# Kernel tuning notes

Hardware: AMD Instinct MI355X
Metric: run time of the kernel (lower is better)

The kernel has to match this reference:

```python
import jax, jax.numpy as jnp
import numpy as np
from jax import lax

B, L = 16, 2048
D_TOK, D_TIS = 256, 64
D_MODEL = D_TOK + D_TIS          # 320
EXPAND = 2
D_INNER = EXPAND * D_MODEL       # 640
D_STATE = 16
D_CONV = 4
DT_RANK = (D_MODEL + 15) // 16   # 20 (ceil(d_model/16), Mamba default)
H_OUT = 128
VOCAB = 65                       # len(CODON_MAP_DNA)+1
N_TISSUES = 30
MAX_NORM = 2.0


def _embed_maxnorm(W, idx):
    # torch nn.Embedding(max_norm=2): looked-up rows are renormalized to norm<=2
    e = W[idx]
    n = jnp.linalg.norm(e, axis=-1, keepdims=True)
    return e * jnp.minimum(1.0, MAX_NORM / jnp.maximum(n, 1e-12))


def setup_inputs() -> dict:
    key = jax.random.key(0)
    ks = jax.random.split(key, 18)
    s = 0.02
    seq_W = jax.random.normal(ks[3], (VOCAB, D_TOK), dtype=jnp.float32)
    seq_W = seq_W.at[0].set(0.0)  # padding_idx=0
    A_log = jnp.log(jnp.broadcast_to(jnp.arange(1, D_STATE + 1, dtype=jnp.float32), (D_INNER, D_STATE)))
    return {
        "rna_data_pad": jax.random.randint(ks[0], (B, L), 0, VOCAB).astype(jnp.int32),
        "tissue_id": jax.random.randint(ks[1], (B,), 0, N_TISSUES).astype(jnp.int32),
        "seq_lengths": jax.random.randint(ks[2], (B,), 1, L + 1).astype(jnp.int32),
        "seq_W": seq_W,
        "tissue_W": jax.random.normal(ks[4], (N_TISSUES, D_TIS), dtype=jnp.float32),
        "in_proj_W": jax.random.normal(ks[5], (2 * D_INNER, D_MODEL), dtype=jnp.float32) * s,
        "conv_w": jax.random.normal(ks[6], (D_INNER, 1, D_CONV), dtype=jnp.float32) * s,
        "conv_b": jnp.zeros((D_INNER,), dtype=jnp.float32),
        "x_proj_W": jax.random.normal(ks[7], (DT_RANK + 2 * D_STATE, D_INNER), dtype=jnp.float32) * s,
        "dt_proj_W": jax.random.normal(ks[8], (D_INNER, DT_RANK), dtype=jnp.float32) * s,
        "dt_proj_b": jax.random.uniform(ks[9], (D_INNER,), minval=-4.0, maxval=-2.0),
        "A_log": A_log,
        "D_skip": jnp.ones((D_INNER,), dtype=jnp.float32),
        "out_proj_W": jax.random.normal(ks[10], (D_MODEL, D_INNER), dtype=jnp.float32) * s,
        "p1_W": jax.random.normal(ks[11], (H_OUT, D_MODEL), dtype=jnp.float32) * s,
        "p1_b": jnp.zeros((H_OUT,), dtype=jnp.float32),
        "p2_W": jax.random.normal(ks[12], (1, H_OUT), dtype=jnp.float32) * s,
        "p2_b": jnp.zeros((1,), dtype=jnp.float32),
    }


def reference(rna_data_pad, tissue_id, seq_lengths, seq_W, tissue_W, in_proj_W,
              conv_w, conv_b, x_proj_W, dt_proj_W, dt_proj_b, A_log, D_skip,
              out_proj_W, p1_W, p1_b, p2_W, p2_b):
    b, l = rna_data_pad.shape
    # embeddings + tissue broadcast + mask
    seq_emb = _embed_maxnorm(seq_W, rna_data_pad)            # [B,L,D_TOK]
    tis_emb = _embed_maxnorm(tissue_W, tissue_id)            # [B,D_TIS]
    tis_exp = jnp.broadcast_to(tis_emb[:, None, :], (b, l, tis_emb.shape[-1]))
    x = jnp.concatenate([seq_emb, tis_exp], axis=-1)          # [B,L,D_MODEL]
    x = x * (rna_data_pad != 0)[..., None]
    # Mamba block
    xz = x @ in_proj_W.T                                      # [B,L,2*D_INNER]
    xm, z = jnp.split(xz, 2, axis=-1)
    xt = xm.transpose(0, 2, 1)                                # [B,D_INNER,L]
    conv = lax.conv_general_dilated(
        xt, conv_w, window_strides=(1,), padding=[(D_CONV - 1, 0)],
        feature_group_count=D_INNER,
        dimension_numbers=("NCH", "OIH", "NCH")) + conv_b[None, :, None]
    xm = jax.nn.silu(conv).transpose(0, 2, 1)                 # [B,L,D_INNER]
    x_dbl = xm @ x_proj_W.T                                   # [B,L,DT_RANK+2*D_STATE]
    dt, Bm, Cm = jnp.split(x_dbl, [DT_RANK, DT_RANK + D_STATE], axis=-1)
    delta = jax.nn.softplus(dt @ dt_proj_W.T + dt_proj_b)     # [B,L,D_INNER]
    A = -jnp.exp(A_log)                                       # [D_INNER,D_STATE]
    # selective scan over time
    xs = (delta.transpose(1, 0, 2), Bm.transpose(1, 0, 2),
          Cm.transpose(1, 0, 2), xm.transpose(1, 0, 2))
    h0 = jnp.zeros((b, D_INNER, D_STATE), dtype=xm.dtype)

    def step(h, t):
        dl, bt, ct, ut = t                                    # [B,di],[B,ds],[B,ds],[B,di]
        dA = jnp.exp(dl[:, :, None] * A)                      # [B,di,ds]
        dBu = (dl * ut)[:, :, None] * bt[:, None, :]          # [B,di,ds]
        h = dA * h + dBu
        y = jnp.einsum("bds,bs->bd", h, ct)
        return h, y

    _, ys = lax.scan(step, h0, xs)                            # ys: [L,B,D_INNER]
    y = ys.transpose(1, 0, 2) + xm * D_skip
    y = y * jax.nn.silu(z)
    out = y @ out_proj_W.T                                    # [B,L,D_MODEL]
    # gather last valid timestep
    out_last = out[jnp.arange(b), seq_lengths - 1]            # [B,D_MODEL]
    h1 = jax.nn.relu(out_last @ p1_W.T + p1_b)
    return h1 @ p2_W.T + p2_b                                 # [B,1]
```

## Files before the change

### kernel.cpp

```cpp
#include <hip/hip_runtime.h>
#include <hip/hip_bf16.h>
#include <hip/hip_fp16.h>
#include <math.h>

#define B_      16
#define L_      2048
#define D_MODEL 320
#define D_INNER 640
#define D_STATE 16
#define DT_RANK 20
#define H_OUT   128
#define VOCAB   65
#define N_TIS   30
#define TT      8
#define ST      64
#define NCHUNK  16
#define CHLEN   (L_/NCHUNK)

static constexpr size_t OFF_MSEQ  = 0;
static constexpr size_t OFF_MTIS  = OFF_MSEQ + VOCAB*1280;
static constexpr size_t OFF_YSCAN = OFF_MTIS + N_TIS*1280;
static constexpr size_t OFF_CLAST = OFF_YSCAN + B_*D_INNER;
static constexpr size_t OFF_XD20  = OFF_CLAST + B_*16;
static constexpr size_t OFF_BBAR  = OFF_XD20 + (size_t)B_*L_*20;
static constexpr size_t OFF_PC    = OFF_BBAR + (size_t)B_*D_STATE*L_;
static constexpr size_t OFF_SC    = OFF_PC + (size_t)B_*NCHUNK*40*256;
static constexpr size_t OFF_U     = OFF_SC + (size_t)B_*NCHUNK*40*256;
static constexpr size_t WS_NEED_BYTES = OFF_U*4 + (size_t)B_*L_*D_INNER*2;

__device__ __forceinline__ float fast_rcp(float x) { return __builtin_amdgcn_rcpf(x); }
__device__ __forceinline__ float silu_f(float x) { return x * fast_rcp(1.0f + __expf(-x)); }

__global__ __launch_bounds__(256) void k_mbuild(
    const float* __restrict__ seqW, const float* __restrict__ tisW,
    const float* __restrict__ inW, float* __restrict__ ws)
{
    __shared__ float a_l[256];
    __shared__ float red[4];
    int v = blockIdx.x, tid = threadIdx.x;
    int K, wofs; const float* src; float* dstM;
    if (v < VOCAB) { K = 256; wofs = 0;   src = seqW + (size_t)v*256;        dstM = ws + OFF_MSEQ + (size_t)v*1280; }
    else           { K = 64;  wofs = 256; src = tisW + (size_t)(v-VOCAB)*64; dstM = ws + OFF_MTIS + (size_t)(v-VOCAB)*1280; }
    float x = (tid < K) ? src[tid] : 0.0f;
    float ss = x * x;
    #pragma unroll
    for (int o = 32; o; o >>= 1) ss += __shfl_xor(ss, o);
    if ((tid & 63) == 0) red[tid >> 6] = ss;
    __syncthreads();
    float tot = red[0] + red[1] + red[2] + red[3];
    float scale = fminf(1.0f, 2.0f / fmaxf(sqrtf(tot), 1e-12f));
    a_l[tid] = (tid < K) ? x * scale : 0.0f;
    __syncthreads();

    int wv = tid >> 6, l = tid & 63;
    float4 a4 = ((const float4*)a_l)[l];
    int j0 = blockIdx.y * 256 + wv * 64;
    bool lane_on = (4*l < K);
    for (int jj = 0; jj < 64; jj += 4) {
        float p[4];
        #pragma unroll
        for (int u = 0; u < 4; ++u) {
            float pv = 0.0f;
            if (lane_on) {
                const float4 w4 = *(const float4*)(inW + (size_t)(j0 + jj + u)*320 + wofs + 4*l);
                pv = a4.x*w4.x + a4.y*w4.y + a4.z*w4.z + a4.w*w4.w;
            }
            p[u] = pv;
        }
        float ta, tb;
        ta=__shfl_xor(p[0],1); tb=__shfl_xor(p[1],1); p[0]=(l&1)?(p[1]+tb):(p[0]+ta);
        ta=__shfl_xor(p[2],1); tb=__shfl_xor(p[3],1); p[2]=(l&1)?(p[3]+tb):(p[2]+ta);
        ta=__shfl_xor(p[0],2); tb=__shfl_xor(p[2],2); p[0]=(l&2)?(p[2]+tb):(p[0]+ta);
        p[0]+=__shfl_xor(p[0],4);  p[0]+=__shfl_xor(p[0],8);
        p[0]+=__shfl_xor(p[0],16); p[0]+=__shfl_xor(p[0],32);
        if (l < 4) dstM[j0 + jj + l] = p[0];
    }
}

__global__ __launch_bounds__(256) void k_xdbl(
    const int* __restrict__ idx, const int* __restrict__ tissue_id,
    const int* __restrict__ seq_lengths,
    const float* __restrict__ conv_w, const float* __restrict__ conv_b,
    const float* __restrict__ xW, float* __restrict__ ws, int use_u)
{
    __shared__ float u_l[TT*641];
    __shared__ float xd_l[TT*36];
    __shared__ int   idx_l[TT+3];
    int b = blockIdx.y;
    int t0 = blockIdx.x * TT;
    int t_last = seq_lengths[b] - 1;
    if (t0 > t_last) return;
    int tid = threadIdx.x;
    const float* Mseq = ws + OFF_MSEQ;
    const float* Mtis = ws + OFF_MTIS;
    int tis = tissue_id[b];
    if (tid < TT+3) {
        int t = t0 - 3 + tid;
        idx_l[tid] = (t >= 0) ? idx[b*L_ + t] : 0;
    }
    __syncthreads();

    for (int d = tid; d < D_INNER; d += 256) {
        float w0 = conv_w[d*4+0], w1 = conv_w[d*4+1], w2 = conv_w[d*4+2], w3 = conv_w[d*4+3];
        float cb = conv_b[d];
        float mt = Mtis[(size_t)tis*1280 + d];
        float xzv[TT+3];
        #pragma unroll
        for (int k = 0; k < TT+3; ++k) {
            unsigned ro = (unsigned)idx_l[k] * 1280u;
            xzv[k] = ro ? (Mseq[ro + (unsigned)d] + mt) : 0.0f;
        }
        #pragma unroll
        for (int t = 0; t < TT; ++t) {
            float c = cb;
            c = fmaf(w0, xzv[t+0], c);
            c = fmaf(w1, xzv[t+1], c);
            c = fmaf(w2, xzv[t+2], c);
            c = fmaf(w3, xzv[t+3], c);
            u_l[t*641 + d] = silu_f(c);
        }
    }
    __syncthreads();

    if (use_u) {
        int nt = min(TT, t_last - t0 + 1);
        __half* Ub = (__half*)(ws + OFF_U) + ((size_t)b*L_ + t0)*D_INNER;
        int cnt = nt * D_INNER;
        for (int o = tid; o < cnt; o += 256) {
            int t = o / D_INNER, d = o - t*D_INNER;
            Ub[o] = __float2half(u_l[t*641 + d]);
        }
    }

    {
        int w = tid >> 6, l = tid & 63;
        float wreg[9][10];
        #pragma unroll
        for (int kk = 0; kk < 9; ++kk) {
            const float* xr = xW + (size_t)(w + 4*kk)*D_INNER + l;
            #pragma unroll
            for (int i = 0; i < 10; ++i) wreg[kk][i] = xr[64*i];
        }
        for (int t = 0; t < TT; ++t) {
            float p[9];
            #pragma unroll
            for (int kk = 0; kk < 9; ++kk) p[kk] = 0.f;
            #pragma unroll
            for (int i = 0; i < 10; ++i) {
                float ui = u_l[t*641 + l + 64*i];
                #pragma unroll
                for (int kk = 0; kk < 9; ++kk) p[kk] = fmaf(wreg[kk][i], ui, p[kk]);
            }
            {
                float ta, tb;
                ta=__shfl_xor(p[0],1); tb=__shfl_xor(p[1],1); p[0]=(l&1)?(p[1]+tb):(p[0]+ta);
                ta=__shfl_xor(p[2],1); tb=__shfl_xor(p[3],1); p[2]=(l&1)?(p[3]+tb):(p[2]+ta);
                ta=__shfl_xor(p[4],1); tb=__shfl_xor(p[5],1); p[4]=(l&1)?(p[5]+tb):(p[4]+ta);
                ta=__shfl_xor(p[6],1); tb=__shfl_xor(p[7],1); p[6]=(l&1)?(p[7]+tb):(p[6]+ta);
                p[8]+=__shfl_xor(p[8],1);
                ta=__shfl_xor(p[0],2); tb=__shfl_xor(p[2],2); p[0]=(l&2)?(p[2]+tb):(p[0]+ta);
                ta=__shfl_xor(p[4],2); tb=__shfl_xor(p[6],2); p[4]=(l&2)?(p[6]+tb):(p[4]+ta);
                p[8]+=__shfl_xor(p[8],2);
                ta=__shfl_xor(p[0],4); tb=__shfl_xor(p[4],4); p[0]=(l&4)?(p[4]+tb):(p[0]+ta);
                p[8]+=__shfl_xor(p[8],4);
                ta=__shfl_xor(p[0],8); tb=__shfl_xor(p[8],8); p[0]=(l&8)?(p[8]+tb):(p[0]+ta);
                p[0]+=__shfl_xor(p[0],16);
                p[0]+=__shfl_xor(p[0],32);
            }
            if (l < 9) xd_l[t*36 + w + 4*l] = p[0];
        }
        if (t_last < t0 + TT) {
            int tl = t_last - t0;
            float pc[4];
            #pragma unroll
            for (int k = 0; k < 4; ++k) pc[k] = 0.f;
            #pragma unroll
            for (int i = 0; i < 10; ++i) {
                float ui = u_l[tl*641 + l + 64*i];
                #pragma unroll
                for (int k = 0; k < 4; ++k)
                    pc[k] = fmaf(xW[(size_t)(36 + w + 4*k)*D_INNER + l + 64*i], ui, pc[k]);
            }
            #pragma unroll
            for (int o = 32; o; o >>= 1) {
                #pragma unroll
                for (int k = 0; k < 4; ++k) pc[k] += __shfl_xor(pc[k], o);
            }
            if (l == 0) {
                #pragma unroll
                for (int k = 0; k < 4; ++k) ws[OFF_CLAST + b*16 + w + 4*k] = pc[k];
            }
        }
    }
    __syncthreads();

    {
        int nt = min(TT, t_last - t0 + 1);
        int cnt = nt * 20;
        float* dst = ws + OFF_XD20 + ((size_t)b*L_ + t0)*20;
        for (int o = tid; o < cnt; o += 256) {
            int t = o / 20, r = o - t*20;
            dst[o] = xd_l[t*36 + r];
        }
        int cntB = nt * 16;
        if (tid < cntB) {
            int s, tt;
            if (nt == TT) { s = tid >> 3; tt = tid & 7; }
            else          { s = tid / nt; tt = tid - s*nt; }
            ws[OFF_BBAR + ((size_t)b*D_STATE + s)*L_ + t0 + tt] = xd_l[tt*36 + 20 + s];
        }
    }
}

__global__ __launch_bounds__(256) void k_scanc(
    const int* __restrict__ idx, const int* __restrict__ tissue_id,
    const int* __restrict__ seq_lengths,
    const float* __restrict__ conv_w, const float* __restrict__ conv_b,
    const float* __restrict__ dtW, const float* __restrict__ dtb,
    const float* __restrict__ A_log, float* __restrict__ ws, int use_u)
{
    __shared__ float xd_t[ST*20];
    __shared__ float dl_t[16*68];
    __shared__ float du_t[16*68];
    __shared__ float Bb_t[16*68];
    __shared__ float sdred[16*17];
    __shared__ int   idx_t[ST+3];

    int dg = blockIdx.x, b = blockIdx.y, c = blockIdx.z;
    int t_last = seq_lengths[b] - 1;
    int t_begin = c * CHLEN;
    if (t_begin > t_last) return;
    int t_end = min(t_begin + CHLEN - 1, t_last);
    int tid = threadIdx.x;
    int dl = tid >> 4, s = tid & 15;
    int dd = tid & 15, tg = tid >> 4;
    int d_own = dg*16 + dd;
    unsigned dco = (unsigned)d_own;
    int tis = tissue_id[b];
    const float* Mseq = ws + OFF_MSEQ;

    float dtw_r[20];
    #pragma unroll
    for (int i = 0; i < 20; i += 4) {
        float4 w4 = *(const float4*)(dtW + d_own*20 + i);
        dtw_r[i] = w4.x; dtw_r[i+1] = w4.y; dtw_r[i+2] = w4.z; dtw_r[i+3] = w4.w;
    }
    float4 cw4 = make_float4(0.f,0.f,0.f,0.f);
    float  cb = 0.f, mt = 0.f;
    if (!use_u) {
        cw4 = *(const float4*)(conv_w + d_own*4);
        cb  = conv_b[d_own];
        mt  = ws[OFF_MTIS + (size_t)tis*1280 + d_own];
    }
    float  dtb_v = dtb[d_own];
    float As = -__expf(A_log[(dg*16 + dl)*D_STATE + s]) * 1.44269504089f;

    float h = 0.0f;
    float sdp = 0.0f;
    for (int t0 = t_begin; t0 <= t_end; t0 += ST) {
        int nt = min(ST, t_end - t0 + 1);
        if (!use_u && tid < ST+3) {
            int t = t0 - 3 + tid;
            idx_t[tid] = (t >= 0 && t < L_) ? idx[b*L_ + t] : 0;
        }
        {
            const float4* src = (const float4*)(ws + OFF_XD20 + ((size_t)b*L_ + t0)*20);
            float4* dst = (float4*)xd_t;
            int cnt4 = nt * 5;
            for (int o = tid; o < cnt4; o += 256) dst[o] = src[o];
        }
        {
            int lr = tid >> 4, c4 = (tid & 15) * 4;
            if (c4 < nt)
                *(float4*)(Bb_t + lr*68 + c4) =
                    *(const float4*)(ws + OFF_BBAR + ((size_t)b*D_STATE + lr)*L_ + t0 + c4);
        }
        __syncthreads();

        {
            int ttb = tg * 4;
            if (ttb < nt) {
                float uu[4];
                if (use_u) {
                    const __half* Ub = (const __half*)(ws + OFF_U)
                                     + ((size_t)b*L_ + t0 + ttb)*D_INNER + dco;
                    #pragma unroll
                    for (int j = 0; j < 4; ++j)
                        uu[j] = (ttb + j < nt) ? __half2float(Ub[(size_t)j*D_INNER]) : 0.0f;
                } else {
                    float xz[7];
                    #pragma unroll
                    for (int k = 0; k < 7; ++k) {
                        unsigned ro = (unsigned)idx_t[ttb + k] * 1280u;
                        xz[k] = ro ? (Mseq[ro + dco] + mt) : 0.0f;
                    }
                    #pragma unroll
                    for (int j = 0; j < 4; ++j) {
                        float cc = cb;
                        cc = fmaf(cw4.x, xz[j+0], cc);
                        cc = fmaf(cw4.y, xz[j+1], cc);
                        cc = fmaf(cw4.z, xz[j+2], cc);
                        cc = fmaf(cw4.w, xz[j+3], cc);
                        uu[j] = (ttb + j < nt) ? silu_f(cc) : 0.0f;
                    }
                }
                float dl4[4], du4[4];
                bool full = (ttb + 3 < nt);
                #pragma unroll
                for (int j = 0; j < 4; ++j) {
                    int tt = ttb + j;
                    if (full || tt < nt) {
                        const float* xr = xd_t + tt*20;
                        float x = dtb_v;
                        #pragma unroll
                        for (int r = 0; r < 20; r += 4) {
                            float4 x4 = *(const float4*)(xr + r);
                            x = fmaf(x4.x, dtw_r[r+0], x);
                            x = fmaf(x4.y, dtw_r[r+1], x);
                            x = fmaf(x4.z, dtw_r[r+2], x);
                            x = fmaf(x4.w, dtw_r[r+3], x);
                        }
                        float e = __expf(-fabsf(x));
                        float sp = fmaxf(x, 0.0f) + __logf(1.0f + e);
                        dl4[j] = sp;
                        du4[j] = sp * uu[j];
                        sdp += sp;
                    } else { dl4[j] = 0.f; du4[j] = 0.f; }
                }
                if (full) {
                    *(float4*)(dl_t + dd*68 + ttb) = make_float4(dl4[0], dl4[1], dl4[2], dl4[3]);
                    *(float4*)(du_t + dd*68 + ttb) = make_float4(du4[0], du4[1], du4[2], du4[3]);
                } else {
                    for (int j = 0; j < 4 && ttb + j < nt; ++j) {
                        dl_t[dd*68 + ttb + j] = dl4[j];
                        du_t[dd*68 + ttb + j] = du4[j];
                    }
                }
            }
        }
        __syncthreads();

        {
            int q4 = nt >> 2;
            #pragma unroll 8
            for (int q = 0; q < q4; ++q) {
                float4 d4 = *(const float4*)(dl_t + dl*68 + 4*q);
                float4 u4 = *(const float4*)(du_t + dl*68 + 4*q);
                float4 b4 = *(const float4*)(Bb_t + s*68 + 4*q);
                float e0 = exp2f(d4.x*As), e1 = exp2f(d4.y*As);
                float e2 = exp2f(d4.z*As), e3 = exp2f(d4.w*As);
                float c0 = u4.x*b4.x, c1 = u4.y*b4.y;
                float c2 = u4.z*b4.z, c3 = u4.w*b4.w;
                h = fmaf(e0, h, c0); h = fmaf(e1, h, c1);
                h = fmaf(e2, h, c2); h = fmaf(e3, h, c3);
            }
            for (int tt = q4*4; tt < nt; ++tt) {
                float dlt = dl_t[dl*68 + tt];
                h = fmaf(exp2f(dlt * As), h, du_t[dl*68 + tt] * Bb_t[s*68 + tt]);
            }
        }
        __syncthreads();
    }
    sdred[tg*17 + dd] = sdp;
    __syncthreads();
    float sd = 0.0f;
    #pragma unroll
    for (int g = 0; g < 16; ++g) sd += sdred[g*17 + dl];
    float P = exp2f(As * sd);
    size_t base = (((size_t)b*NCHUNK + c)*40 + dg)*256 + tid;
    ws[OFF_PC + base] = P;
    ws[OFF_SC + base] = h;
}

__global__ __launch_bounds__(256) void k_comb(const int* __restrict__ seq_lengths,
                                              float* __restrict__ ws)
{
    int b = blockIdx.y, dg = blockIdx.x;
    int tid = threadIdx.x;
    int dl = tid >> 4, s = tid & 15;
    int t_last = seq_lengths[b] - 1;
    int ncv = t_last / CHLEN + 1;
    float h = 0.0f;
    for (int c = 0; c < ncv; ++c) {
        size_t base = (((size_t)b*NCHUNK + c)*40 + dg)*256 + tid;
        h = fmaf(ws[OFF_PC + base], h, ws[OFF_SC + base]);
    }
    float v = h * ws[OFF_CLAST + b*16 + s];
    v += __shfl_xor(v, 1); v += __shfl_xor(v, 2);
    v += __shfl_xor(v, 4); v += __shfl_xor(v, 8);
    if (s == 0) ws[OFF_YSCAN + (size_t)b*D_INNER + dg*16 + dl] = v;
}

__global__ __launch_bounds__(1024) void k_final(
    const int* __restrict__ idx, const int* __restrict__ tissue_id,
    const int* __restrict__ seq_lengths,
    const float* __restrict__ conv_w, const float* __restrict__ conv_b,
    const float* __restrict__ Dskip, const float* __restrict__ outW,
    const float* __restrict__ p1W, const float* __restrict__ p1b,
    const float* __restrict__ p2W, const float* __restrict__ p2b,
    const float* __restrict__ ws, float* __restrict__ out)
{
    __shared__ float y_l[D_INNER];
    __shared__ float o_l[D_MODEL];
    __shared__ float h1_l[H_OUT];
    int b = blockIdx.x, tid = threadIdx.x;
    int t_last = seq_lengths[b] - 1;
    int tis = tissue_id[b];
    const float* Mseq = ws + OFF_MSEQ;
    const float* Mtis = ws + OFF_MTIS;
    int rows[4];
    #pragma unroll
    for (int k = 0; k < 4; ++k) {
        int t = t_last - 3 + k;
        rows[k] = (t >= 0) ? idx[b*L_ + t] : 0;
    }
    if (tid < D_INNER) {
        int d = tid;
        float conv = conv_b[d];
        const float* cw = conv_w + d*4;
        #pragma unroll
        for (int k = 0; k < 4; ++k) {
            unsigned ro = (unsigned)rows[k] * 1280u;
            float xzv = ro ? (Mseq[ro + (unsigned)d] + Mtis[(size_t)tis*1280 + d]) : 0.0f;
            conv += cw[k] * xzv;
        }
        float u = silu_f(conv);
        unsigned roL = (unsigned)rows[3] * 1280u;
        float z = roL ? (Mseq[roL + 640u + (unsigned)d] + Mtis[(size_t)tis*1280 + 640 + d]) : 0.0f;
        float ys = ws[OFF_YSCAN + (size_t)b*D_INNER + d];
        y_l[d] = (ys + u * Dskip[d]) * silu_f(z);
    }
    __syncthreads();
    {
        int j = tid >> 1, half = tid & 1;
        float acc = 0.f;
        if (j < D_MODEL) {
            const float* w = outW + (size_t)j*D_INNER + half*320;
            const float* y = y_l + half*320;
            #pragma unroll 4
            for (int k = 0; k < 320; k += 4) {
                float4 w4 = *(const float4*)(w + k);
                acc += y[k]*w4.x + y[k+1]*w4.y + y[k+2]*w4.z + y[k+3]*w4.w;
            }
        }
        acc += __shfl_xor(acc, 1);
        if (j < D_MODEL && half == 0) o_l[j] = acc;
    }
    __syncthreads();
    {
        int j = tid >> 3, part = tid & 7;
        float acc = 0.f;
        if (j < H_OUT) {
            const float* w = p1W + (size_t)j*D_MODEL + part*40;
            const float* o = o_l + part*40;
            #pragma unroll
            for (int k = 0; k < 40; k += 4) {
                float4 w4 = *(const float4*)(w + k);
                acc += o[k]*w4.x + o[k+1]*w4.y + o[k+2]*w4.z + o[k+3]*w4.w;
            }
        }
        acc += __shfl_xor(acc, 1); acc += __shfl_xor(acc, 2); acc += __shfl_xor(acc, 4);
        if (j < H_OUT && part == 0) h1_l[j] = fmaxf(acc + p1b[j], 0.0f);
    }
    __syncthreads();
    if (tid < 64) {
        float v = h1_l[tid]*p2W[tid] + h1_l[tid+64]*p2W[tid+64];
        v += __shfl_xor(v, 32); v += __shfl_xor(v, 16); v += __shfl_xor(v, 8);
        v += __shfl_xor(v, 4);  v += __shfl_xor(v, 2);  v += __shfl_xor(v, 1);
        if (tid == 0) out[b] = v + p2b[0];
    }
}

extern "C" void kernel_launch(void* const* d_in, const int* in_sizes, int n_in,
                              void* d_out, int out_size, void* d_ws, size_t ws_size,
                              hipStream_t stream)
{
    const int*   idx   = (const int*)d_in[0];
    const int*   tis   = (const int*)d_in[1];
    const int*   slen  = (const int*)d_in[2];
    const float* seqW  = (const float*)d_in[3];
    const float* tisW  = (const float*)d_in[4];
    const float* inW   = (const float*)d_in[5];
    const float* convw = (const float*)d_in[6];
    const float* convb = (const float*)d_in[7];
    const float* xW    = (const float*)d_in[8];
    const float* dtW   = (const float*)d_in[9];
    const float* dtb   = (const float*)d_in[10];
    const float* Alog  = (const float*)d_in[11];
    const float* Dsk   = (const float*)d_in[12];
    const float* outW  = (const float*)d_in[13];
    const float* p1W   = (const float*)d_in[14];
    const float* p1b   = (const float*)d_in[15];
    const float* p2W   = (const float*)d_in[16];
    const float* p2b   = (const float*)d_in[17];
    float* ws  = (float*)d_ws;
    float* out = (float*)d_out;

    int use_u = (ws_size >= WS_NEED_BYTES) ? 1 : 0;

    hipLaunchKernelGGL(k_mbuild, dim3(VOCAB + N_TIS, 5), dim3(256), 0, stream, seqW, tisW, inW, ws);
    hipLaunchKernelGGL(k_xdbl,   dim3(L_/TT, B_),        dim3(256), 0, stream,
                       idx, tis, slen, convw, convb, xW, ws, use_u);
    hipLaunchKernelGGL(k_scanc,  dim3(D_INNER/16, B_, NCHUNK), dim3(256), 0, stream,
                       idx, tis, slen, convw, convb, dtW, dtb, Alog, ws, use_u);
    hipLaunchKernelGGL(k_comb,   dim3(D_INNER/16, B_),   dim3(256), 0, stream, slen, ws);
    hipLaunchKernelGGL(k_final,  dim3(B_),               dim3(1024), 0, stream,
                       idx, tis, slen, convw, convb, Dsk, outW, p1W, p1b, p2W, p2b, ws, out);
}
```

Measured before the change: 244.8 us.

## Add reverse-time closed-form scan exploiting A=-(1..16) structure with runtime check

Adds a check kernel that verifies A_log rows equal log(1..16). When it passes, a new per-channel scan kernel runs instead of the old one. The new kernel walks each chunk backwards from its end and weights contributions by integer powers of exp(-cumulative delta), so no per-state exponentials or cross-thread reductions are needed. The combine step rebuilds per-state decays from the same powers. The fp16 u buffer path is removed and B is also stored time-major; the general path remains as a fallback at the cost of an extra launch and extra flag-dependent kernel launches.

```diff
diff --git a/kernel.cpp b/kernel.cpp
--- a/kernel.cpp
+++ b/kernel.cpp
@@ -1,6 +1,5 @@
 #include <hip/hip_runtime.h>
 #include <hip/hip_bf16.h>
-#include <hip/hip_fp16.h>
 #include <math.h>
 
 #define B_      16
@@ -16,20 +15,46 @@
 #define ST      64
 #define NCHUNK  16
 #define CHLEN   (L_/NCHUNK)
+#define NCH2    32
+#define CHL2    (L_/NCH2)
 
 static constexpr size_t OFF_MSEQ  = 0;
-static constexpr size_t OFF_MTIS  = OFF_MSEQ + VOCAB*1280;
-static constexpr size_t OFF_YSCAN = OFF_MTIS + N_TIS*1280;
+static constexpr size_t OFF_MTIS  = OFF_MSEQ  + VOCAB*1280;
+static constexpr size_t OFF_YSCAN = OFF_MTIS  + N_TIS*1280;
 static constexpr size_t OFF_CLAST = OFF_YSCAN + B_*D_INNER;
-static constexpr size_t OFF_XD20  = OFF_CLAST + B_*16;
+static constexpr size_t OFF_FLAG  = OFF_CLAST + B_*16;
+static constexpr size_t OFF_XD20  = OFF_FLAG  + 16;
 static constexpr size_t OFF_BBAR  = OFF_XD20 + (size_t)B_*L_*20;
-static constexpr size_t OFF_PC    = OFF_BBAR + (size_t)B_*D_STATE*L_;
-static constexpr size_t OFF_SC    = OFF_PC + (size_t)B_*NCHUNK*40*256;
-static constexpr size_t OFF_U     = OFF_SC + (size_t)B_*NCHUNK*40*256;
-static constexpr size_t WS_NEED_BYTES = OFF_U*4 + (size_t)B_*L_*D_INNER*2;
+static constexpr size_t OFF_BT    = OFF_BBAR + (size_t)B_*D_STATE*L_;
+static constexpr size_t OFF_PC    = OFF_BT   + (size_t)B_*L_*D_STATE;
+static constexpr size_t OFF_SC    = OFF_PC   + (size_t)B_*NCHUNK*40*256;
+static constexpr size_t OFF_PCN   = OFF_SC   + (size_t)B_*NCHUNK*40*256;
+static constexpr size_t OFF_SCN   = OFF_PCN  + (size_t)B_*NCH2*D_INNER;
 
 __device__ __forceinline__ float fast_rcp(float x) { return __builtin_amdgcn_rcpf(x); }
 __device__ __forceinline__ float silu_f(float x) { return x * fast_rcp(1.0f + __expf(-x)); }
+
+__global__ __launch_bounds__(256) void k_check(const float* __restrict__ A_log,
+                                               float* __restrict__ ws)
+{
+    __shared__ int oksh;
+    int tid = threadIdx.x;
+    if (tid == 0) oksh = 1;
+    __syncthreads();
+    int ok = 1;
+    for (int i = tid; i < D_INNER*D_STATE; i += 256) {
+        int s = i & 15;
+        float v = A_log[i];
+        if (v != A_log[s]) ok = 0;
+        if (i < 16) {
+            float a = __expf(v);
+            if (fabsf(a - (float)(s+1)) > 1e-3f*(float)(s+1)) ok = 0;
+        }
+    }
+    if (!ok) atomicAnd(&oksh, 0);
+    __syncthreads();
+    if (tid == 0) ((int*)ws)[OFF_FLAG] = oksh;
+}
 
 __global__ __launch_bounds__(256) void k_mbuild(
     const float* __restrict__ seqW, const float* __restrict__ tisW,
@@ -81,7 +106,7 @@
     const int* __restrict__ idx, const int* __restrict__ tissue_id,
     const int* __restrict__ seq_lengths,
     const float* __restrict__ conv_w, const float* __restrict__ conv_b,
-    const float* __restrict__ xW, float* __restrict__ ws, int use_u)
+    const float* __restrict__ xW, float* __restrict__ ws)
 {
     __shared__ float u_l[TT*641];
     __shared__ float xd_l[TT*36];
@@ -121,16 +146,6 @@
         }
     }
     __syncthreads();
-
-    if (use_u) {
-        int nt = min(TT, t_last - t0 + 1);
-        __half* Ub = (__half*)(ws + OFF_U) + ((size_t)b*L_ + t0)*D_INNER;
-        int cnt = nt * D_INNER;
-        for (int o = tid; o < cnt; o += 256) {
-            int t = o / D_INNER, d = o - t*D_INNER;
-            Ub[o] = __float2half(u_l[t*641 + d]);
-        }
-    }
 
     {
         int w = tid >> 6, l = tid & 63;
@@ -209,7 +224,119 @@
             else          { s = tid / nt; tt = tid - s*nt; }
             ws[OFF_BBAR + ((size_t)b*D_STATE + s)*L_ + t0 + tt] = xd_l[tt*36 + 20 + s];
         }
-    }
+        for (int o = tid; o < cntB; o += 256) {
+            int t = o >> 4, s = o & 15;
+            ws[OFF_BT + ((size_t)b*L_ + t0 + t)*16 + s] = xd_l[t*36 + 20 + s];
+        }
+    }
+}
+
+__global__ __launch_bounds__(128) void k_scan2(
+    const int* __restrict__ idx, const int* __restrict__ tissue_id,
+    const int* __restrict__ seq_lengths,
+    const float* __restrict__ conv_w, const float* __restrict__ conv_b,
+    const float* __restrict__ dtW, const float* __restrict__ dtb,
+    float* __restrict__ ws)
+{
+    if (((const int*)ws)[OFF_FLAG] == 0) return;
+    int b = blockIdx.y, c = blockIdx.z;
+    int t_last = seq_lengths[b] - 1;
+    int t_begin = c * CHL2;
+    if (t_begin > t_last) return;
+    int t_end = min(t_begin + CHL2 - 1, t_last);
+    int d = blockIdx.x * 128 + threadIdx.x;
+    unsigned du = (unsigned)d;
+    int tis = tissue_id[b];
+    const float* Mseq = ws + OFF_MSEQ;
+    const float* xd   = ws + OFF_XD20 + (size_t)b*L_*20;
+    const float* BT   = ws + OFF_BT   + (size_t)b*L_*16;
+    const int*   idxb = idx + b*L_;
+
+    float dtw_r[20];
+    #pragma unroll
+    for (int i = 0; i < 20; i += 4) {
+        float4 w4 = *(const float4*)(dtW + d*20 + i);
+        dtw_r[i] = w4.x; dtw_r[i+1] = w4.y; dtw_r[i+2] = w4.z; dtw_r[i+3] = w4.w;
+    }
+    float4 cw4 = *(const float4*)(conv_w + d*4);
+    float  cb  = conv_b[d];
+    float  dtb_v = dtb[d];
+    float  mt  = ws[OFF_MTIS + (size_t)tis*1280 + d];
+    const float L2E = 1.44269504089f;
+
+    float xw0, xw1, xw2, xw3;
+    {
+        int t;
+        t = t_end;     { int row = idxb[t]; xw3 = row ? (Mseq[(unsigned)row*1280u + du] + mt) : 0.f; }
+        t = t_end - 1; { float v = 0.f; if (t >= 0) { int row = idxb[t]; v = row ? (Mseq[(unsigned)row*1280u + du] + mt) : 0.f; } xw2 = v; }
+        t = t_end - 2; { float v = 0.f; if (t >= 0) { int row = idxb[t]; v = row ? (Mseq[(unsigned)row*1280u + du] + mt) : 0.f; } xw1 = v; }
+        t = t_end - 3; { float v = 0.f; if (t >= 0) { int row = idxb[t]; v = row ? (Mseq[(unsigned)row*1280u + du] + mt) : 0.f; } xw0 = v; }
+    }
+
+    float h[16];
+    #pragma unroll
+    for (int s = 0; s < 16; ++s) h[s] = 0.f;
+    float r = 0.f;
+
+    for (int t = t_end; t >= t_begin; --t) {
+        float cc = cb;
+        cc = fmaf(cw4.x, xw0, cc);
+        cc = fmaf(cw4.y, xw1, cc);
+        cc = fmaf(cw4.z, xw2, cc);
+        cc = fmaf(cw4.w, xw3, cc);
+        float u = silu_f(cc);
+        const float4* xr4 = (const float4*)(xd + (size_t)t*20);
+        float x = dtb_v;
+        #pragma unroll
+        for (int q = 0; q < 5; ++q) {
+            float4 x4 = xr4[q];
+            x = fmaf(x4.x, dtw_r[4*q+0], x);
+            x = fmaf(x4.y, dtw_r[4*q+1], x);
+            x = fmaf(x4.z, dtw_r[4*q+2], x);
+            x = fmaf(x4.w, dtw_r[4*q+3], x);
+        }
+        float e  = __expf(-fabsf(x));
+        float dl = fmaxf(x, 0.0f) + __logf(1.0f + e);
+        float F  = dl * u;
+        float p1 = exp2f(-L2E * r);
+        float p2 = p1*p1, p3 = p2*p1, p4 = p2*p2;
+        float p5 = p4*p1, p6 = p4*p2, p7 = p4*p3, p8 = p4*p4;
+        float p9 = p8*p1, p10 = p8*p2, p11 = p8*p3, p12 = p8*p4;
+        float p13 = p8*p5, p14 = p8*p6, p15 = p8*p7, p16 = p8*p8;
+        const float4* Bt4 = (const float4*)(BT + (size_t)t*16);
+        float4 B0 = Bt4[0], B1 = Bt4[1], B2 = Bt4[2], B3 = Bt4[3];
+        h[0]  = fmaf(F*B0.x, p1,  h[0]);
+        h[1]  = fmaf(F*B0.y, p2,  h[1]);
+        h[2]  = fmaf(F*B0.z, p3,  h[2]);
+        h[3]  = fmaf(F*B0.w, p4,  h[3]);
+        h[4]  = fmaf(F*B1.x, p5,  h[4]);
+        h[5]  = fmaf(F*B1.y, p6,  h[5]);
+        h[6]  = fmaf(F*B1.z, p7,  h[6]);
+        h[7]  = fmaf(F*B1.w, p8,  h[7]);
+        h[8]  = fmaf(F*B2.x, p9,  h[8]);
+        h[9]  = fmaf(F*B2.y, p10, h[9]);
+        h[10] = fmaf(F*B2.z, p11, h[10]);
+        h[11] = fmaf(F*B2.w, p12, h[11]);
+        h[12] = fmaf(F*B3.x, p13, h[12]);
+        h[13] = fmaf(F*B3.y, p14, h[13]);
+        h[14] = fmaf(F*B3.z, p15, h[14]);
+        h[15] = fmaf(F*B3.w, p16, h[15]);
+        r += dl;
+        xw3 = xw2; xw2 = xw1; xw1 = xw0;
+        {
+            int tn = t - 4;
+            float v = 0.f;
+            if (tn >= 0) { int row = idxb[tn]; v = row ? (Mseq[(unsigned)row*1280u + du] + mt) : 0.f; }
+            xw0 = v;
+        }
+    }
+
+    ws[OFF_PCN + ((size_t)b*NCH2 + c)*D_INNER + d] = exp2f(-L2E * r);
+    float* dst = ws + OFF_SCN + (((size_t)b*NCH2 + c)*D_INNER + d)*16;
+    ((float4*)dst)[0] = make_float4(h[0],  h[1],  h[2],  h[3]);
+    ((float4*)dst)[1] = make_float4(h[4],  h[5],  h[6],  h[7]);
+    ((float4*)dst)[2] = make_float4(h[8],  h[9],  h[10], h[11]);
+    ((float4*)dst)[3] = make_float4(h[12], h[13], h[14], h[15]);
 }
 
 __global__ __launch_bounds__(256) void k_scanc(
@@ -217,8 +344,9 @@
     const int* __restrict__ seq_lengths,
     const float* __restrict__ conv_w, const float* __restrict__ conv_b,
     const float* __restrict__ dtW, const float* __restrict__ dtb,
-    const float* __restrict__ A_log, float* __restrict__ ws, int use_u)
-{
+    const float* __restrict__ A_log, float* __restrict__ ws)
+{
+    if (((const int*)ws)[OFF_FLAG] != 0) return;
     __shared__ float xd_t[ST*20];
     __shared__ float dl_t[16*68];
     __shared__ float du_t[16*68];
@@ -245,21 +373,17 @@
         float4 w4 = *(const float4*)(dtW + d_own*20 + i);
         dtw_r[i] = w4.x; dtw_r[i+1] = w4.y; dtw_r[i+2] = w4.z; dtw_r[i+3] = w4.w;
     }
-    float4 cw4 = make_float4(0.f,0.f,0.f,0.f);
-    float  cb = 0.f, mt = 0.f;
-    if (!use_u) {
-        cw4 = *(const float4*)(conv_w + d_own*4);
-        cb  = conv_b[d_own];
-        mt  = ws[OFF_MTIS + (size_t)tis*1280 + d_own];
-    }
+    float4 cw4 = *(const float4*)(conv_w + d_own*4);
+    float  cb  = conv_b[d_own];
     float  dtb_v = dtb[d_own];
+    float  mt  = ws[OFF_MTIS + (size_t)tis*1280 + d_own];
     float As = -__expf(A_log[(dg*16 + dl)*D_STATE + s]) * 1.44269504089f;
 
     float h = 0.0f;
     float sdp = 0.0f;
     for (int t0 = t_begin; t0 <= t_end; t0 += ST) {
         int nt = min(ST, t_end - t0 + 1);
-        if (!use_u && tid < ST+3) {
+        if (tid < ST+3) {
             int t = t0 - 3 + tid;
             idx_t[tid] = (t >= 0 && t < L_) ? idx[b*L_ + t] : 0;
         }
@@ -280,29 +404,11 @@
         {
             int ttb = tg * 4;
             if (ttb < nt) {
-                float uu[4];
-                if (use_u) {
-                    const __half* Ub = (const __half*)(ws + OFF_U)
-                                     + ((size_t)b*L_ + t0 + ttb)*D_INNER + dco;
-                    #pragma unroll
-                    for (int j = 0; j < 4; ++j)
-                        uu[j] = (ttb + j < nt) ? __half2float(Ub[(size_t)j*D_INNER]) : 0.0f;
-                } else {
-                    float xz[7];
-                    #pragma unroll
-                    for (int k = 0; k < 7; ++k) {
-                        unsigned ro = (unsigned)idx_t[ttb + k] * 1280u;
-                        xz[k] = ro ? (Mseq[ro + dco] + mt) : 0.0f;
-                    }
-                    #pragma unroll
-                    for (int j = 0; j < 4; ++j) {
-                        float cc = cb;
-                        cc = fmaf(cw4.x, xz[j+0], cc);
-                        cc = fmaf(cw4.y, xz[j+1], cc);
-                        cc = fmaf(cw4.z, xz[j+2], cc);
-                        cc = fmaf(cw4.w, xz[j+3], cc);
-                        uu[j] = (ttb + j < nt) ? silu_f(cc) : 0.0f;
-                    }
+                float xz[7];
+                #pragma unroll
+                for (int k = 0; k < 7; ++k) {
+                    unsigned ro = (unsigned)idx_t[ttb + k] * 1280u;
+                    xz[k] = ro ? (Mseq[ro + dco] + mt) : 0.0f;
                 }
                 float dl4[4], du4[4];
                 bool full = (ttb + 3 < nt);
@@ -310,20 +416,26 @@
                 for (int j = 0; j < 4; ++j) {
                     int tt = ttb + j;
                     if (full || tt < nt) {
+                        float cc = cb;
+                        cc = fmaf(cw4.x, xz[j+0], cc);
+                        cc = fmaf(cw4.y, xz[j+1], cc);
+                        cc = fmaf(cw4.z, xz[j+2], cc);
+                        cc = fmaf(cw4.w, xz[j+3], cc);
+                        float u = silu_f(cc);
                         const float* xr = xd_t + tt*20;
                         float x = dtb_v;
                         #pragma unroll
-                        for (int r = 0; r < 20; r += 4) {
-                            float4 x4 = *(const float4*)(xr + r);
-                            x = fmaf(x4.x, dtw_r[r+0], x);
-                            x = fmaf(x4.y, dtw_r[r+1], x);
-                            x = fmaf(x4.z, dtw_r[r+2], x);
-                            x = fmaf(x4.w, dtw_r[r+3], x);
+                        for (int rr = 0; rr < 20; rr += 4) {
+                            float4 x4 = *(const float4*)(xr + rr);
+                            x = fmaf(x4.x, dtw_r[rr+0], x);
+                            x = fmaf(x4.y, dtw_r[rr+1], x);
+                            x = fmaf(x4.z, dtw_r[rr+2], x);
+                            x = fmaf(x4.w, dtw_r[rr+3], x);
                         }
                         float e = __expf(-fabsf(x));
                         float sp = fmaxf(x, 0.0f) + __logf(1.0f + e);
                         dl4[j] = sp;
-                        du4[j] = sp * uu[j];
+                        du4[j] = sp * u;
                         sdp += sp;
                     } else { dl4[j] = 0.f; du4[j] = 0.f; }
                 }
@@ -379,11 +491,29 @@
     int tid = threadIdx.x;
     int dl = tid >> 4, s = tid & 15;
     int t_last = seq_lengths[b] - 1;
-    int ncv = t_last / CHLEN + 1;
+    int flag = ((const int*)ws)[OFF_FLAG];
     float h = 0.0f;
-    for (int c = 0; c < ncv; ++c) {
-        size_t base = (((size_t)b*NCHUNK + c)*40 + dg)*256 + tid;
-        h = fmaf(ws[OFF_PC + base], h, ws[OFF_SC + base]);
+    if (flag) {
+        int d = dg*16 + dl;
+        int n = s + 1;
+        int ncv = t_last / CHL2 + 1;
+        for (int c = 0; c < ncv; ++c) {
+            float Es = ws[OFF_PCN + ((size_t)b*NCH2 + c)*D_INNER + d];
+            float e2 = Es*Es, e4 = e2*e2, e8 = e4*e4, e16 = e8*e8;
+            float W = (n & 1) ? Es : 1.0f;
+            W *= (n & 2)  ? e2  : 1.0f;
+            W *= (n & 4)  ? e4  : 1.0f;
+            W *= (n & 8)  ? e8  : 1.0f;
+            W *= (n & 16) ? e16 : 1.0f;
+            float Sc = ws[OFF_SCN + (((size_t)b*NCH2 + c)*D_INNER + d)*16 + s];
+            h = fmaf(W, h, Sc);
+        }
+    } else {
+        int ncv = t_last / CHLEN + 1;
+        for (int c = 0; c < ncv; ++c) {
+            size_t base = (((size_t)b*NCHUNK + c)*40 + dg)*256 + tid;
+            h = fmaf(ws[OFF_PC + base], h, ws[OFF_SC + base]);
+        }
     }
     float v = h * ws[OFF_CLAST + b*16 + s];
     v += __shfl_xor(v, 1); v += __shfl_xor(v, 2);
@@ -496,13 +626,14 @@
     float* ws  = (float*)d_ws;
     float* out = (float*)d_out;
 
-    int use_u = (ws_size >= WS_NEED_BYTES) ? 1 : 0;
-
+    hipLaunchKernelGGL(k_check,  dim3(1),               dim3(256), 0, stream, Alog, ws);
     hipLaunchKernelGGL(k_mbuild, dim3(VOCAB + N_TIS, 5), dim3(256), 0, stream, seqW, tisW, inW, ws);
     hipLaunchKernelGGL(k_xdbl,   dim3(L_/TT, B_),        dim3(256), 0, stream,
-                       idx, tis, slen, convw, convb, xW, ws, use_u);
+                       idx, tis, slen, convw, convb, xW, ws);
+    hipLaunchKernelGGL(k_scan2,  dim3(D_INNER/128, B_, NCH2), dim3(128), 0, stream,
+                       idx, tis, slen, convw, convb, dtW, dtb, ws);
     hipLaunchKernelGGL(k_scanc,  dim3(D_INNER/16, B_, NCHUNK), dim3(256), 0, stream,
-                       idx, tis, slen, convw, convb, dtW, dtb, Alog, ws, use_u);
+                       idx, tis, slen, convw, convb, dtW, dtb, Alog, ws);
     hipLaunchKernelGGL(k_comb,   dim3(D_INNER/16, B_),   dim3(256), 0, stream, slen, ws);
     hipLaunchKernelGGL(k_final,  dim3(B_),               dim3(1024), 0, stream,
                        idx, tis, slen, convw, convb, Dsk, outW, p1W, p1b, p2W, p2b, ws, out);
```

New measurement: 273.3 us. +11.7%, slower.
